# Kernel optimization log

Measured on AMD Instinct MI355X. Metric: run time of the kernel, lower is better.

Reference implementation:

```python
import jax, jax.numpy as jnp
import numpy as np

N, P, E, D, T, R, K = 4096, 32768, 4096, 128, 3, 4, 16
CURRENT_TIME = 1.0


def setup_inputs() -> dict:
    key = jax.random.key(0)
    ks = jax.random.split(key, 12)
    pairs = jax.random.randint(ks[0], (P, 2), 0, N)
    adj = (jax.random.randint(ks[1], (N, N), 0, 100) == 0).astype(jnp.int32)
    adj = jnp.maximum(adj, adj.T) * (1 - jnp.eye(N, dtype=jnp.int32))
    neigh_idx = jax.random.randint(ks[2], (N, R, K), 0, N)
    node_type = jax.random.randint(ks[3], (N,), 0, T)
    # event timestamps far in the past so the decay sum stays O(1)
    t_events = -(jax.random.uniform(ks[4], (E,), dtype=jnp.float32) * 100.0 + 50.0)
    node_embeds = 0.1 * jax.random.normal(ks[5], (N, D), dtype=jnp.float32)
    W_proj = 0.1 * jax.random.normal(ks[6], (T, D, D), dtype=jnp.float32)
    W_beta = 0.1 * jax.random.normal(ks[7], (R, D, D), dtype=jnp.float32)
    b_beta = 0.1 * jax.random.normal(ks[8], (R, D), dtype=jnp.float32)
    decay_theta = jnp.float32(0.1)
    q1 = jnp.float32(0.5)
    q2 = jnp.float32(0.1)
    return dict(pairs=pairs, adj=adj, neigh_idx=neigh_idx, node_type=node_type,
                t_events=t_events, node_embeds=node_embeds, W_proj=W_proj,
                W_beta=W_beta, b_beta=b_beta, decay_theta=decay_theta, q1=q1, q2=q2)


def _forward(pairs, adj, neigh_idx, node_type, t_events, node_embeds,
             W_proj, W_beta, b_beta, decay_theta, q1, q2):
    n_nodes, d = node_embeds.shape
    adj_f = adj.astype(node_embeds.dtype)
    pm, pn = pairs[:, 0], pairs[:, 1]

    # --- HistoricalEdgeModule: type-specific projection + global decay sum ---
    proj_all = jnp.einsum('nd,tde->tne', node_embeds, W_proj)      # [T,N,D]
    proj = proj_all[node_type, jnp.arange(n_nodes)]                # [N,D]
    diff = proj[pm] - proj[pn]
    gamma_base = -jnp.sqrt(jnp.sum(diff * diff, axis=-1))          # [P]
    sum_alpha = jnp.sum(jnp.exp(-decay_theta * (CURRENT_TIME - t_events)))
    lambda_hist = gamma_base + sum_alpha                           # [P]

    # --- TriadicClosureModule: clustering coeff + common-neighbor sum ---
    deg = adj_f.sum(axis=1)
    tri = jnp.sum((adj_f @ adj_f) * adj_f.T, axis=1)               # diag(A^3)
    denom = deg * (deg - 1.0)
    denom = jnp.where(denom == 0, 1e-6, denom)
    C = 2.0 * tri / denom                                          # [N]
    common = adj_f[pm] * adj_f[pn]                                 # [P,N] common-neighbor mask
    Csum = common @ C                                              # [P]
    g = -jnp.sum((node_embeds[pm] - node_embeds[pn]) ** 2, axis=-1)
    lambda_tri = Csum * g                                          # [P]

    # --- NeighborInfluenceModule: per-relation mean agg -> macro sigmoid ---
    h_r = node_embeds[neigh_idx].mean(axis=2)                      # [N,R,D]
    h_agg = jnp.einsum('nrd,rde->nre', h_r, W_beta) + b_beta       # [N,R,D]
    eps = jax.nn.sigmoid(h_agg.mean(axis=1))                       # [N,D]
    lambda_neigh = jnp.sum(eps[pm] * eps[pn], axis=-1) / d         # [P]

    lam = jnp.exp(lambda_hist + lambda_tri + lambda_neigh)
    return jax.nn.sigmoid(q1 * lam + q2)


def reference(pairs, adj, neigh_idx, node_type, t_events, node_embeds,
              W_proj, W_beta, b_beta, decay_theta, q1, q2):
    return _forward(pairs, adj, neigh_idx, node_type, t_events, node_embeds,
                    W_proj, W_beta, b_beta, decay_theta, q1, q2)
```

## Files before the change

kernel.cpp:

```cpp
#include <hip/hip_runtime.h>
#include <math.h>

#define N_NODES 4096
#define DIM     128
#define NPAIRS  32768
#define NEVENTS 4096
#define NTYPES  3
#define NREL    4
#define NNEIGH  16
#define WORDS   64
#define MAXDEG  192


typedef int nt_int4 __attribute__((ext_vector_type(4)));

#define PA_MASK_END  (N_NODES * 4)
#define PA_PROJ_END  (PA_MASK_END + N_NODES)
#define PA_HR_END    (PA_PROJ_END + N_NODES * NREL * DIM / (256 * 4))
#define PA_TOTAL     (PA_HR_END + 1)

__global__ __launch_bounds__(256) void k_phaseA(const int* __restrict__ adj,
                                                unsigned long long* __restrict__ mask,
                                                const float* __restrict__ x,
                                                const int* __restrict__ ntype,
                                                const float* __restrict__ Wp,
                                                float* __restrict__ proj,
                                                const int* __restrict__ nidx,
                                                float* __restrict__ h,
                                                const float* __restrict__ t_events,
                                                const float* __restrict__ theta_p,
                                                float* __restrict__ salpha) {
    __shared__ __align__(16) float smem[1280];
    int b = blockIdx.x;

    if (b < PA_MASK_END) {
        int row = b >> 2;
        int q   = b & 3;
        int wave = threadIdx.x >> 6;
        int lane = threadIdx.x & 63;
        const nt_int4* arow = (const nt_int4*)(adj + (size_t)row * N_NODES);
        nt_int4 v = __builtin_nontemporal_load(&arow[q * 256 + wave * 64 + lane]);
        unsigned long long b0 = __ballot(v.x != 0);
        unsigned long long b1 = __ballot(v.y != 0);
        unsigned long long b2 = __ballot(v.z != 0);
        unsigned long long b3 = __ballot(v.w != 0);
        if (lane < 4) {
            unsigned long long w = (lane == 0) ? b0 : (lane == 1) ? b1 : (lane == 2) ? b2 : b3;
            mask[(size_t)row * WORDS + (q * 4 + wave) * 4 + lane] = w;
        }

    } else if (b < PA_PROJ_END) {
        int n = b - PA_MASK_END;
        int eg = threadIdx.x & 31;
        int kg = threadIdx.x >> 5;
        float* xs = smem;
        float* part = smem + 128;
        if (threadIdx.x < 32)
            ((float4*)xs)[threadIdx.x] = ((const float4*)(x + (size_t)n * DIM))[threadIdx.x];
        __syncthreads();
        int t = ntype[n];
        const float4* W4 = (const float4*)(Wp + (size_t)t * DIM * DIM) + eg;
        float4 acc = {0.f, 0.f, 0.f, 0.f};
        int k0 = kg * 16;
        #pragma unroll
        for (int kk = 0; kk < 16; ++kk) {
            float xk = xs[k0 + kk];
            float4 w = W4[(size_t)(k0 + kk) * 32];
            acc.x += xk * w.x; acc.y += xk * w.y; acc.z += xk * w.z; acc.w += xk * w.w;
        }
        ((float4*)(part + kg * 128))[eg] = acc;
        __syncthreads();
        if (threadIdx.x < 128) {
            int e = threadIdx.x;
            float s = part[e] + part[128 + e] + part[256 + e] + part[384 + e]
                    + part[512 + e] + part[640 + e] + part[768 + e] + part[896 + e];
            proj[(size_t)n * DIM + e] = s;
        }

    } else if (b < PA_HR_END) {
        int tid = (b - PA_PROJ_END) * 256 + threadIdx.x;
        int dq = tid & 31;
        int nr = tid >> 5;
        const int4* idx4 = (const int4*)(nidx + (size_t)nr * NNEIGH);
        int4 i0 = idx4[0], i1 = idx4[1], i2 = idx4[2], i3 = idx4[3];
        const float4* xb = (const float4*)x;
        float4 s = {0.f, 0.f, 0.f, 0.f};
        float4 v;
        #define ACC4(i) v = xb[(size_t)(i) * 32 + dq]; s.x += v.x; s.y += v.y; s.z += v.z; s.w += v.w;
        ACC4(i0.x) ACC4(i0.y) ACC4(i0.z) ACC4(i0.w)
        ACC4(i1.x) ACC4(i1.y) ACC4(i1.z) ACC4(i1.w)
        ACC4(i2.x) ACC4(i2.y) ACC4(i2.z) ACC4(i2.w)
        ACC4(i3.x) ACC4(i3.y) ACC4(i3.z) ACC4(i3.w)
        #undef ACC4
        float4 r;
        r.x = s.x * (1.0f / 16.0f); r.y = s.y * (1.0f / 16.0f);
        r.z = s.z * (1.0f / 16.0f); r.w = s.w * (1.0f / 16.0f);
        ((float4*)h)[(size_t)nr * 32 + dq] = r;

    } else {
        float th = theta_p[0];
        float acc = 0.f;
        for (int i = threadIdx.x; i < NEVENTS; i += 256)
            acc += expf(-th * (1.0f - t_events[i]));
        smem[threadIdx.x] = acc;
        __syncthreads();
        for (int s = 128; s > 0; s >>= 1) {
            if (threadIdx.x < s) smem[threadIdx.x] += smem[threadIdx.x + s];
            __syncthreads();
        }
        if (threadIdx.x == 0) salpha[0] = smem[0];
    }
}

__global__ __launch_bounds__(256) void k_clust(const unsigned long long* __restrict__ mask,
                                               float* __restrict__ C) {
    __shared__ unsigned short nl[MAXDEG];
    __shared__ unsigned int wacc[4];
    __shared__ int sdeg;
    int node = blockIdx.x;
    int wave = threadIdx.x >> 6;
    int lane = threadIdx.x & 63;
    unsigned long long my = mask[(size_t)node * WORDS + lane];

    if (wave == 0) {
        int pc = (int)__popcll(my);
        int scan = pc;
        #pragma unroll
        for (int off = 1; off < 64; off <<= 1) {
            int nv = __shfl_up(scan, off);
            if (lane >= off) scan += nv;
        }
        int excl = scan - pc;
        if (lane == 63) sdeg = scan;
        int jb = (lane >> 2) * 256 + (lane & 3);
        unsigned long long ww = my;
        int o = excl;
        while (ww) {
            int bit = __ffsll(ww) - 1;
            if (o < MAXDEG) nl[o] = (unsigned short)(jb + bit * 4);
            ++o;
            ww &= ww - 1;
        }
    }
    __syncthreads();
    int dg = sdeg;
    int pidx = wave + 4 * lane;
    int pre = (lane < 48) ? (int)nl[pidx] : 0;
    int nit = (dg - wave + 3) >> 2;
    if (nit < 0) nit = 0;
    unsigned int acc = 0;
    #pragma unroll 4
    for (int t = 0; t < nit; ++t) {
        int j = __shfl(pre, t);
        acc += __popcll(my & mask[(size_t)j * WORDS + lane]);
    }
    for (int off = 32; off > 0; off >>= 1) acc += __shfl_xor(acc, off);
    if (lane == 0) wacc[wave] = acc;
    __syncthreads();
    if (threadIdx.x == 0) {
        float tri = (float)(wacc[0] + wacc[1] + wacc[2] + wacc[3]);
        float dgF = (float)dg;
        float denom = dgF * (dgF - 1.0f);
        if (denom == 0.0f) denom = 1e-6f;
        C[node] = 2.0f * tri / denom;
    }
}

__global__ __launch_bounds__(256) void k_eps(const float* __restrict__ h,
                                             const float* __restrict__ Wb,
                                             const float* __restrict__ bb,
                                             float* __restrict__ eps) {
    __shared__ float hs[4 * 512];
    __shared__ float part[8 * 4 * 128];
    int base = blockIdx.x * 4;
    int eg = threadIdx.x & 31;
    int g  = threadIdx.x >> 5;
    int e0 = eg * 4;

    const float4* hsrc = (const float4*)(h + (size_t)base * NREL * DIM);
    float4* hs4 = (float4*)hs;
    hs4[threadIdx.x]       = hsrc[threadIdx.x];
    hs4[threadIdx.x + 256] = hsrc[threadIdx.x + 256];
    __syncthreads();

    const float* W = Wb + (size_t)(g * 64) * DIM + e0;
    float4 a0 = {0,0,0,0}, a1 = {0,0,0,0}, a2 = {0,0,0,0}, a3 = {0,0,0,0};
    int hq = g * 16;
    #pragma unroll 2
    for (int kk = 0; kk < 16; ++kk) {
        float4 h0 = hs4[0 * 128 + hq + kk];
        float4 h1 = hs4[1 * 128 + hq + kk];
        float4 h2 = hs4[2 * 128 + hq + kk];
        float4 h3 = hs4[3 * 128 + hq + kk];
        float4 w0 = *(const float4*)&W[(size_t)(kk * 4 + 0) * DIM];
        float4 w1 = *(const float4*)&W[(size_t)(kk * 4 + 1) * DIM];
        float4 w2 = *(const float4*)&W[(size_t)(kk * 4 + 2) * DIM];
        float4 w3 = *(const float4*)&W[(size_t)(kk * 4 + 3) * DIM];
        a0.x += h0.x*w0.x + h0.y*w1.x + h0.z*w2.x + h0.w*w3.x;
        a0.y += h0.x*w0.y + h0.y*w1.y + h0.z*w2.y + h0.w*w3.y;
        a0.z += h0.x*w0.z + h0.y*w1.z + h0.z*w2.z + h0.w*w3.z;
        a0.w += h0.x*w0.w + h0.y*w1.w + h0.z*w2.w + h0.w*w3.w;
        a1.x += h1.x*w0.x + h1.y*w1.x + h1.z*w2.x + h1.w*w3.x;
        a1.y += h1.x*w0.y + h1.y*w1.y + h1.z*w2.y + h1.w*w3.y;
        a1.z += h1.x*w0.z + h1.y*w1.z + h1.z*w2.z + h1.w*w3.z;
        a1.w += h1.x*w0.w + h1.y*w1.w + h1.z*w2.w + h1.w*w3.w;
        a2.x += h2.x*w0.x + h2.y*w1.x + h2.z*w2.x + h2.w*w3.x;
        a2.y += h2.x*w0.y + h2.y*w1.y + h2.z*w2.y + h2.w*w3.y;
        a2.z += h2.x*w0.z + h2.y*w1.z + h2.z*w2.z + h2.w*w3.z;
        a2.w += h2.x*w0.w + h2.y*w1.w + h2.z*w2.w + h2.w*w3.w;
        a3.x += h3.x*w0.x + h3.y*w1.x + h3.z*w2.x + h3.w*w3.x;
        a3.y += h3.x*w0.y + h3.y*w1.y + h3.z*w2.y + h3.w*w3.y;
        a3.z += h3.x*w0.z + h3.y*w1.z + h3.z*w2.z + h3.w*w3.z;
        a3.w += h3.x*w0.w + h3.y*w1.w + h3.z*w2.w + h3.w*w3.w;
    }
    float4* p4 = (float4*)part;
    p4[(g * 4 + 0) * 32 + eg] = a0;
    p4[(g * 4 + 1) * 32 + eg] = a1;
    p4[(g * 4 + 2) * 32 + eg] = a2;
    p4[(g * 4 + 3) * 32 + eg] = a3;
    __syncthreads();
    #pragma unroll
    for (int rep = 0; rep < 2; ++rep) {
        int idx = threadIdx.x + rep * 256;
        int m = idx >> 7;
        int e = idx & 127;
        float s = 0.f;
        #pragma unroll
        for (int gg = 0; gg < 8; ++gg)
            s += part[(gg * 4 + m) * 128 + e];
        float bsum = bb[e] + bb[DIM + e] + bb[2 * DIM + e] + bb[3 * DIM + e];
        float v = (s + bsum) * 0.25f;
        eps[(size_t)(base + m) * DIM + e] = 1.0f / (1.0f + expf(-v));
    }
}

__global__ __launch_bounds__(256) void k_pairs(const int* __restrict__ pairs,
                                               const unsigned long long* __restrict__ mask,
                                               const float* __restrict__ C,
                                               const float* __restrict__ proj,
                                               const float* __restrict__ eps,
                                               const float* __restrict__ x,
                                               const float* __restrict__ salpha_p,
                                               const float* __restrict__ q1p,
                                               const float* __restrict__ q2p,
                                               float* __restrict__ out) {
    int wave = threadIdx.x >> 6;
    int lane = threadIdx.x & 63;
    int p = blockIdx.x * 4 + wave;
    int pm = pairs[p * 2];
    int pn = pairs[p * 2 + 1];

    unsigned long long cw = mask[(size_t)pm * WORDS + lane] & mask[(size_t)pn * WORDS + lane];
    float csum = 0.f;
    int jbase = (lane >> 2) * 256 + (lane & 3);
    while (cw) {
        int bit = __ffsll(cw) - 1;
        csum += C[jbase + bit * 4];
        cw &= cw - 1;
    }

    const float2* Am = (const float2*)(proj + (size_t)pm * DIM);
    const float2* An = (const float2*)(proj + (size_t)pn * DIM);
    const float2* Xm = (const float2*)(x    + (size_t)pm * DIM);
    const float2* Xn = (const float2*)(x    + (size_t)pn * DIM);
    const float2* Em = (const float2*)(eps  + (size_t)pm * DIM);
    const float2* En = (const float2*)(eps  + (size_t)pn * DIM);
    float2 am = Am[lane], an = An[lane];
    float2 xm = Xm[lane], xn = Xn[lane];
    float2 em = Em[lane], en = En[lane];

    float dpx = am.x - an.x, dpy = am.y - an.y;
    float s1 = dpx * dpx + dpy * dpy;
    float dxx = xm.x - xn.x, dxy = xm.y - xn.y;
    float s2 = dxx * dxx + dxy * dxy;
    float s3 = em.x * en.x + em.y * en.y;

    for (int off = 32; off > 0; off >>= 1) {
        s1 += __shfl_xor(s1, off);
        s2 += __shfl_xor(s2, off);
        s3 += __shfl_xor(s3, off);
        csum += __shfl_xor(csum, off);
    }
    if (lane == 0) {
        float lhist  = -sqrtf(s1) + salpha_p[0];
        float ltri   = csum * (-s2);
        float lneigh = s3 * (1.0f / 128.0f);
        float lam = expf(lhist + ltri + lneigh);
        float z = q1p[0] * lam + q2p[0];
        out[p] = 1.0f / (1.0f + expf(-z));
    }
}

extern "C" void kernel_launch(void* const* d_in, const int* in_sizes, int n_in,
                              void* d_out, int out_size, void* d_ws, size_t ws_size,
                              hipStream_t stream) {
    const int*   pairs    = (const int*)d_in[0];
    const int*   adj      = (const int*)d_in[1];
    const int*   nidx     = (const int*)d_in[2];
    const int*   ntype    = (const int*)d_in[3];
    const float* t_events = (const float*)d_in[4];
    const float* x        = (const float*)d_in[5];
    const float* Wp       = (const float*)d_in[6];
    const float* Wb       = (const float*)d_in[7];
    const float* bb       = (const float*)d_in[8];
    const float* theta    = (const float*)d_in[9];
    const float* q1       = (const float*)d_in[10];
    const float* q2       = (const float*)d_in[11];
    float* out = (float*)d_out;

    char* ws = (char*)d_ws;
    unsigned long long* mask = (unsigned long long*)(ws + 0);
    float* C      = (float*)(ws + 2113536);
    float* proj   = (float*)(ws + 2129920);
    float* eps    = (float*)(ws + 4227072);
    float* salpha = (float*)(ws + 6324224);
    float* h      = (float*)(ws + 6324352);

    hipLaunchKernelGGL(k_phaseA, dim3(PA_TOTAL),    dim3(256), 0, stream,
                       adj, mask, x, ntype, Wp, proj, nidx, h, t_events, theta, salpha);
    hipLaunchKernelGGL(k_clust,  dim3(N_NODES),     dim3(256), 0, stream, mask, C);
    hipLaunchKernelGGL(k_eps,    dim3(N_NODES / 4), dim3(256), 0, stream, h, Wb, bb, eps);
    hipLaunchKernelGGL(k_pairs,  dim3(NPAIRS / 4),  dim3(256), 0, stream,
                       pairs, mask, C, proj, eps, x, salpha, q1, q2, out);
}
```

Measured before the change: 83.50 us.

## Build per-segment neighbor lists in mask kernel instead of serial scan in clustering

The adjacency-to-bitmask phase now also emits compact neighbor index lists per 256-column segment, with counts, into workspace. The clustering kernel reads these precomputed lists directly. This removes the single-wave prefix scan, the serial bit extraction and the block barrier that ran before the triangle-counting loop. The cost is extra global writes and reads of the lists. A segment holding more than 32 neighbors would be truncated, since its count is stored but the list stops at 32 entries.

```diff
diff --git a/kernel.cpp b/kernel.cpp
--- a/kernel.cpp
+++ b/kernel.cpp
@@ -9,7 +9,8 @@
 #define NREL    4
 #define NNEIGH  16
 #define WORDS   64
-#define MAXDEG  192
+#define SEGS    16
+#define SEGCAP  32
 
 
 typedef int nt_int4 __attribute__((ext_vector_type(4)));
@@ -21,6 +22,8 @@
 
 __global__ __launch_bounds__(256) void k_phaseA(const int* __restrict__ adj,
                                                 unsigned long long* __restrict__ mask,
+                                                unsigned short* __restrict__ nbrl,
+                                                unsigned short* __restrict__ segcnt,
                                                 const float* __restrict__ x,
                                                 const int* __restrict__ ntype,
                                                 const float* __restrict__ Wp,
@@ -44,9 +47,23 @@
         unsigned long long b1 = __ballot(v.y != 0);
         unsigned long long b2 = __ballot(v.z != 0);
         unsigned long long b3 = __ballot(v.w != 0);
+        int ch = q * 4 + wave;
         if (lane < 4) {
             unsigned long long w = (lane == 0) ? b0 : (lane == 1) ? b1 : (lane == 2) ? b2 : b3;
-            mask[(size_t)row * WORDS + (q * 4 + wave) * 4 + lane] = w;
+            mask[(size_t)row * WORDS + ch * 4 + lane] = w;
+            int p0 = (int)__popcll(b0), p1 = (int)__popcll(b1), p2 = (int)__popcll(b2);
+            int off = (lane > 0 ? p0 : 0) + (lane > 1 ? p1 : 0) + (lane > 2 ? p2 : 0);
+            unsigned short* nl = nbrl + ((size_t)row * SEGS + ch) * SEGCAP;
+            int colbase = ch * 256 + lane;
+            while (w) {
+                int bit = __ffsll(w) - 1;
+                if (off < SEGCAP) nl[off] = (unsigned short)(colbase + bit * 4);
+                ++off;
+                w &= w - 1;
+            }
+            if (lane == 3)
+                segcnt[row * SEGS + ch] =
+                    (unsigned short)(p0 + p1 + p2 + (int)__popcll(b3));
         }
 
     } else if (b < PA_PROJ_END) {
@@ -113,53 +130,45 @@
 }
 
 __global__ __launch_bounds__(256) void k_clust(const unsigned long long* __restrict__ mask,
+                                               const unsigned short* __restrict__ nbrl,
+                                               const unsigned short* __restrict__ segcnt,
                                                float* __restrict__ C) {
-    __shared__ unsigned short nl[MAXDEG];
     __shared__ unsigned int wacc[4];
-    __shared__ int sdeg;
+    __shared__ unsigned int wdeg[4];
     int node = blockIdx.x;
     int wave = threadIdx.x >> 6;
     int lane = threadIdx.x & 63;
     unsigned long long my = mask[(size_t)node * WORDS + lane];
-
-    if (wave == 0) {
-        int pc = (int)__popcll(my);
-        int scan = pc;
-        #pragma unroll
-        for (int off = 1; off < 64; off <<= 1) {
-            int nv = __shfl_up(scan, off);
-            if (lane >= off) scan += nv;
-        }
-        int excl = scan - pc;
-        if (lane == 63) sdeg = scan;
-        int jb = (lane >> 2) * 256 + (lane & 3);
-        unsigned long long ww = my;
-        int o = excl;
-        while (ww) {
-            int bit = __ffsll(ww) - 1;
-            if (o < MAXDEG) nl[o] = (unsigned short)(jb + bit * 4);
-            ++o;
-            ww &= ww - 1;
-        }
-    }
-    __syncthreads();
-    int dg = sdeg;
-    int pidx = wave + 4 * lane;
-    int pre = (lane < 48) ? (int)nl[pidx] : 0;
-    int nit = (dg - wave + 3) >> 2;
-    if (nit < 0) nit = 0;
+    const unsigned short* nl = nbrl + (size_t)node * SEGS * SEGCAP;
+    const unsigned short* sc = segcnt + node * SEGS;
+    int c0 = sc[wave], c1 = sc[4 + wave], c2 = sc[8 + wave], c3 = sc[12 + wave];
+    int pre0 = (lane < 32) ? (int)nl[wave * SEGCAP + lane]
+                           : (int)nl[(4 + wave) * SEGCAP + (lane - 32)];
+    int pre1 = (lane < 32) ? (int)nl[(8 + wave) * SEGCAP + lane]
+                           : (int)nl[(12 + wave) * SEGCAP + (lane - 32)];
     unsigned int acc = 0;
-    #pragma unroll 4
-    for (int t = 0; t < nit; ++t) {
-        int j = __shfl(pre, t);
+    for (int t = 0; t < c0; ++t) {
+        int j = __shfl(pre0, t);
         acc += __popcll(my & mask[(size_t)j * WORDS + lane]);
     }
+    for (int t = 0; t < c1; ++t) {
+        int j = __shfl(pre0, 32 + t);
+        acc += __popcll(my & mask[(size_t)j * WORDS + lane]);
+    }
+    for (int t = 0; t < c2; ++t) {
+        int j = __shfl(pre1, t);
+        acc += __popcll(my & mask[(size_t)j * WORDS + lane]);
+    }
+    for (int t = 0; t < c3; ++t) {
+        int j = __shfl(pre1, 32 + t);
+        acc += __popcll(my & mask[(size_t)j * WORDS + lane]);
+    }
     for (int off = 32; off > 0; off >>= 1) acc += __shfl_xor(acc, off);
-    if (lane == 0) wacc[wave] = acc;
+    if (lane == 0) { wacc[wave] = acc; wdeg[wave] = (unsigned int)(c0 + c1 + c2 + c3); }
     __syncthreads();
     if (threadIdx.x == 0) {
         float tri = (float)(wacc[0] + wacc[1] + wacc[2] + wacc[3]);
-        float dgF = (float)dg;
+        float dgF = (float)(wdeg[0] + wdeg[1] + wdeg[2] + wdeg[3]);
         float denom = dgF * (dgF - 1.0f);
         if (denom == 0.0f) denom = 1e-6f;
         C[node] = 2.0f * tri / denom;
@@ -315,10 +324,13 @@
     float* eps    = (float*)(ws + 4227072);
     float* salpha = (float*)(ws + 6324224);
     float* h      = (float*)(ws + 6324352);
+    unsigned short* nbrl   = (unsigned short*)(ws + 14712960);
+    unsigned short* segcnt = (unsigned short*)(ws + 18907264);
 
     hipLaunchKernelGGL(k_phaseA, dim3(PA_TOTAL),    dim3(256), 0, stream,
-                       adj, mask, x, ntype, Wp, proj, nidx, h, t_events, theta, salpha);
-    hipLaunchKernelGGL(k_clust,  dim3(N_NODES),     dim3(256), 0, stream, mask, C);
+                       adj, mask, nbrl, segcnt, x, ntype, Wp, proj, nidx, h,
+                       t_events, theta, salpha);
+    hipLaunchKernelGGL(k_clust,  dim3(N_NODES),     dim3(256), 0, stream, mask, nbrl, segcnt, C);
     hipLaunchKernelGGL(k_eps,    dim3(N_NODES / 4), dim3(256), 0, stream, h, Wb, bb, eps);
     hipLaunchKernelGGL(k_pairs,  dim3(NPAIRS / 4),  dim3(256), 0, stream,
                        pairs, mask, C, proj, eps, x, salpha, q1, q2, out);
```

Measured after the change: 89.42 us. 1.07x slower.
